# Kernel tuning notes

Hardware: AMD Instinct MI355X
Metric: run time of the kernel (lower is better)

Reference implementation:

```python
import jax, jax.numpy as jnp
import numpy as np

B, L, D, N_HEADS = 8, 512, 1024, 16
D_HEAD = D // N_HEADS


def _mha_fuzzy(x_q, x_k, x_v, Wq, bq, Wk, bk, Wv, bv, Wo, bo):
    """Multi-head fuzzy attention, product t-norm score function."""
    b, lq, d_model = x_q.shape
    lk = x_k.shape[1]

    def proj(x, W, bias, l):
        # [b, l, D] -> [b, h, l, d_head]
        return (x @ W + bias).reshape(b, l, N_HEADS, D_HEAD).transpose(0, 2, 1, 3)

    Q = proj(x_q, Wq, bq, lq)
    K = proj(x_k, Wk, bk, lk)
    V = proj(x_v, Wv, bv, lk)
    # fuzzy memberships in [0,1]
    mu_q = jax.nn.sigmoid(Q)
    mu_k = jax.nn.sigmoid(K)
    # product t-norm aggregated over feature dim (mean), then softmax normalize
    scores = jnp.einsum('bhid,bhjd->bhij', mu_q, mu_k) / D_HEAD  # [b,h,lq,lk]
    attn = jax.nn.softmax(scores, axis=-1)
    out = jnp.einsum('bhij,bhjd->bhid', attn, V)
    out = out.transpose(0, 2, 1, 3).reshape(b, lq, d_model)
    return out @ Wo + bo, attn.mean(axis=1)  # avg over heads


def setup_inputs() -> dict:
    key = jax.random.key(0)
    ks = jax.random.split(key, 16)
    s = 1.0 / np.sqrt(D)
    inp = {
        'text_features': jax.random.normal(ks[0], (B, L, D), jnp.float32),
        'image_features': jax.random.normal(ks[1], (B, L, D), jnp.float32),
        'Wq': jax.random.normal(ks[2], (D, D), jnp.float32) * s,
        'bq': jnp.zeros((D,), jnp.float32),
        'Wk': jax.random.normal(ks[3], (D, D), jnp.float32) * s,
        'bk': jnp.zeros((D,), jnp.float32),
        'Wv': jax.random.normal(ks[4], (D, D), jnp.float32) * s,
        'bv': jnp.zeros((D,), jnp.float32),
        'Wo': jax.random.normal(ks[5], (D, D), jnp.float32) * s,
        'bo': jnp.zeros((D,), jnp.float32),
        'W1': jax.random.normal(ks[6], (3 * D, D), jnp.float32) * (1.0 / np.sqrt(3 * D)),
        'b1': jnp.zeros((D,), jnp.float32),
        'W2': jax.random.normal(ks[7], (D, D), jnp.float32) * s,
        'b2': jnp.zeros((D,), jnp.float32),
    }
    return inp


def reference(text_features, image_features, Wq, bq, Wk, bk, Wv, bv, Wo, bo, W1, b1, W2, b2):
    # shared fuzzy attention module applied in both cross-modal directions
    text_cross, avg_attn = _mha_fuzzy(text_features, image_features, image_features,
                                      Wq, bq, Wk, bk, Wv, bv, Wo, bo)
    image_cross, _ = _mha_fuzzy(image_features, text_features, text_features,
                                Wq, bq, Wk, bk, Wv, bv, Wo, bo)
    combined = jnp.concatenate([text_features, image_features, text_cross], axis=-1)
    hidden = jax.nn.relu(combined @ W1 + b1)
    compositional_output = hidden @ W2 + b2
    return text_cross, image_cross, compositional_output, avg_attn
```

## Files before the change

kernel.cpp:

```cpp
#include <hip/hip_runtime.h>

#define NB 8
#define SL 512
#define DM 1024
#define NH 16
#define DH 64

using bfrag = __attribute__((ext_vector_type(8))) short;
using facc  = __attribute__((ext_vector_type(4))) float;

__device__ __forceinline__ float bf2f(ushort u) {
    return __uint_as_float(((unsigned)u) << 16);
}
__device__ __forceinline__ ushort f2bf(float f) {
    unsigned x = __float_as_uint(f);
    return (ushort)((x + 0x7FFFu + ((x >> 16) & 1u)) >> 16);
}
__device__ __forceinline__ float4 bf4_f4(ushort4 u) {
    return make_float4(bf2f(u.x), bf2f(u.y), bf2f(u.z), bf2f(u.w));
}
__device__ __forceinline__ unsigned pack2(float a, float b) {
    return (unsigned)f2bf(a) | ((unsigned)f2bf(b) << 16);
}
__device__ __forceinline__ void gload16(const ushort* g, ushort* l) {
    __builtin_amdgcn_global_load_lds(
        (const __attribute__((address_space(1))) unsigned*)g,
        (__attribute__((address_space(3))) unsigned*)l, 16, 0, 0);
}

__global__ __launch_bounds__(256)
void cvt_k(const float* __restrict__ s, ushort* __restrict__ d) {
    const size_t i = (size_t)(blockIdx.x * 256 + threadIdx.x) * 4;
    const float4 f = *(const float4*)(s + i);
    *(ushort4*)(d + i) = make_ushort4(f2bf(f.x), f2bf(f.y), f2bf(f.z), f2bf(f.w));
}

__global__ __launch_bounds__(256)
void tconv_k(const float* __restrict__ W, ushort* __restrict__ WT,
             const int R, const int C) {
    __shared__ ushort T[64][68];
    const int tid = threadIdx.x;
    const int c0 = blockIdx.x * 64, r0 = blockIdx.y * 64;
    #pragma unroll
    for (int rr = 0; rr < 4; ++rr) {
        const int r = (tid >> 4) + rr * 16;
        const int c4 = (tid & 15) * 4;
        const float4 f = *(const float4*)(W + (size_t)(r0 + r) * C + c0 + c4);
        T[c4+0][r] = f2bf(f.x); T[c4+1][r] = f2bf(f.y);
        T[c4+2][r] = f2bf(f.z); T[c4+3][r] = f2bf(f.w);
    }
    __syncthreads();
    #pragma unroll
    for (int rr = 0; rr < 4; ++rr) {
        const int c = (tid >> 4) + rr * 16;
        const int r4 = (tid & 15) * 4;
        *(ushort4*)(WT + (size_t)(c0 + c) * R + r0 + r4) =
            make_ushort4(T[c][r4+0], T[c][r4+1], T[c][r4+2], T[c][r4+3]);
    }
}

template<int ACT, int OMODE>
__global__ __launch_bounds__(256, 2)
void mfma_gemm(const ushort* __restrict__ A0, const ushort* __restrict__ A1,
               const float* __restrict__ A2f,
               const int KA1, const int KA2, const int Ktot,
               const int lda, const int ldaf,
               const ushort* __restrict__ AM1, const int Msplit,
               const ushort* __restrict__ BT, const int ldb,
               const float* __restrict__ bias, const float* __restrict__ biasK,
               const float* __restrict__ biasV,
               float* __restrict__ outf, ushort* __restrict__ outb,
               ushort* __restrict__ outbK, ushort* __restrict__ outbVT,
               const int clustN)
{
    __shared__ ushort sh[32768];
    const int tid  = threadIdx.x;
    const int w    = tid >> 6;
    const int lane = tid & 63;
    const int ln   = lane & 15, qd = lane >> 4;
    const int wm = (w & 1) * 64, wn = (w >> 1) * 64;

    const int NTg = gridDim.x, MTg = gridDim.y;
    const int L   = blockIdx.x + NTg * blockIdx.y;
    const int xcd = L & 7, sIdx = L >> 3;
    int mt, nt;
    if (clustN) { const int np = NTg >> 3; nt = xcd * np + sIdx % np; mt = sIdx / np; }
    else        { mt = xcd * (MTg >> 3) + sIdx / NTg; nt = sIdx - (sIdx / NTg) * NTg; }
    const int m0 = mt * 128, n0 = nt * 128;

    const ushort* A0u = A0; const ushort* A1u = A1; int m0A = m0;
    if (Msplit && m0 >= Msplit) { A0u = AM1; A1u = AM1; m0A = m0 - Msplit; }

    const int arow = (lane >> 3);
    const int kc8s = ((lane & 7) ^ arow) * 8;

    facc acc[4][4];
    #pragma unroll
    for (int i = 0; i < 4; ++i)
        #pragma unroll
        for (int j = 0; j < 4; ++j)
            acc[i][j] = (facc){0.f, 0.f, 0.f, 0.f};

    auto stage = [&](int k0, ushort* buf) {
        ushort* Asb = buf;
        ushort* Bsb = buf + 8192;
        #pragma unroll
        for (int t = 0; t < 4; ++t) {
            const int c = w * 4 + t;
            gload16(BT + (size_t)(n0 + c * 8 + arow) * ldb + k0 + kc8s,
                    &Bsb[c * 512]);
        }
        if (k0 < KA2) {
            const ushort* Ab; int ko;
            if (k0 < KA1) { Ab = A0u; ko = k0; }
            else          { Ab = A1u; ko = k0 - KA1; }
            #pragma unroll
            for (int t = 0; t < 4; ++t) {
                const int c = w * 4 + t;
                gload16(Ab + (size_t)(m0A + c * 8 + arow) * lda + ko + kc8s,
                        &Asb[c * 512]);
            }
        } else {
            const int ko = k0 - KA2;
            #pragma unroll
            for (int t = 0; t < 4; ++t) {
                const int c = w * 4 + t;
                const float* src = A2f + (size_t)(m0A + c * 8 + arow) * ldaf + ko + kc8s;
                const float4 f0 = *(const float4*)src;
                const float4 f1 = *(const float4*)(src + 4);
                uint4 p;
                p.x = pack2(f0.x, f0.y); p.y = pack2(f0.z, f0.w);
                p.z = pack2(f1.x, f1.y); p.w = pack2(f1.z, f1.w);
                *(uint4*)&Asb[c * 512 + lane * 8] = p;
            }
        }
    };

    stage(0, sh);
    for (int k0 = 0; k0 < Ktot; k0 += 64) {
        ushort* cur = sh + ((k0 >> 6) & 1) * 16384;
        ushort* nxt = sh + (((k0 >> 6) & 1) ^ 1) * 16384;
        __syncthreads();
        if (k0 + 64 < Ktot) stage(k0 + 64, nxt);
        ushort* Asb = cur;
        ushort* Bsb = cur + 8192;
        #pragma unroll
        for (int ks = 0; ks < 2; ++ks) {
            const int ch = (ks * 4 + qd) ^ (ln & 7);
            bfrag af[4], bfv[4];
            #pragma unroll
            for (int i = 0; i < 4; ++i)
                af[i] = *(const bfrag*)&Asb[(wm + i*16 + ln) * 64 + ch * 8];
            #pragma unroll
            for (int j = 0; j < 4; ++j)
                bfv[j] = *(const bfrag*)&Bsb[(wn + j*16 + ln) * 64 + ch * 8];
            #pragma unroll
            for (int i = 0; i < 4; ++i)
                #pragma unroll
                for (int j = 0; j < 4; ++j)
                    acc[i][j] = __builtin_amdgcn_mfma_f32_16x16x32_bf16(
                        af[i], bfv[j], acc[i][j], 0, 0, 0);
        }
    }

    if (OMODE == 4) {
        const int seg   = n0 >> 10;
        const int nloc0 = n0 & 1023;
        const float* bs = (seg == 0) ? bias : (seg == 1) ? biasK : biasV;
        if (seg < 2) {
            ushort* ob = (seg == 0) ? outb : outbK;
            #pragma unroll
            for (int j = 0; j < 4; ++j) {
                const int nl = nloc0 + wn + j * 16 + ln;
                const float bn = bs[nl];
                #pragma unroll
                for (int i = 0; i < 4; ++i) {
                    const int mb = m0 + wm + i * 16 + qd * 4;
                    #pragma unroll
                    for (int r = 0; r < 4; ++r) {
                        const float v = 1.f / (1.f + __expf(-(acc[i][j][r] + bn)));
                        const int m = mb + r;
                        const int g = m >> 9, l = m & 511;
                        ob[(((size_t)(g * NH + (nl >> 6))) * SL + l) * DH + (nl & 63)]
                            = f2bf(v);
                    }
                }
            }
        } else {
            __syncthreads();
            #pragma unroll
            for (int j = 0; j < 4; ++j) {
                const int n_l = wn + j * 16 + ln;
                const float bn = bs[nloc0 + n_l];
                #pragma unroll
                for (int i = 0; i < 4; ++i) {
                    #pragma unroll
                    for (int r = 0; r < 4; ++r) {
                        const int m_l = wm + i * 16 + qd * 4 + r;
                        const int c = (m_l >> 3) ^ (n_l & 7);
                        sh[n_l * 128 + c * 8 + (m_l & 7)] = f2bf(acc[i][j][r] + bn);
                    }
                }
            }
            __syncthreads();
            const int n_l = tid >> 1, half = tid & 1;
            const int nl = nloc0 + n_l;
            const int g = m0 >> 9, l0 = m0 & 511;
            ushort* dst = outbVT +
                (((size_t)(g * NH + (nl >> 6))) * DH + (nl & 63)) * SL + l0;
            #pragma unroll
            for (int u = 0; u < 8; ++u) {
                const int c = half * 8 + u;
                const int cs = c ^ (n_l & 7);
                *(uint4*)(dst + c * 8) = *(const uint4*)&sh[n_l * 128 + cs * 8];
            }
        }
        return;
    }

    #pragma unroll
    for (int j = 0; j < 4; ++j) {
        const int n = n0 + wn + j * 16 + ln;
        const float bn = bias[n];
        #pragma unroll
        for (int i = 0; i < 4; ++i) {
            const int mb = m0 + wm + i * 16 + qd * 4;
            #pragma unroll
            for (int r = 0; r < 4; ++r) {
                float v = acc[i][j][r] + bn;
                if (ACT == 1)      v = 1.f / (1.f + __expf(-v));
                else if (ACT == 2) v = v > 0.f ? v : 0.f;
                const int m = mb + r;
                if (OMODE == 0) outf[(size_t)m * DM + n] = v;
                else            outb[(size_t)m * DM + n] = f2bf(v);
            }
        }
    }
}

__global__ __launch_bounds__(256, 2)
void attn2_k(const ushort* __restrict__ Qm, const ushort* __restrict__ Km,
             const ushort* __restrict__ VTm, ushort* __restrict__ AO,
             float* __restrict__ RS)
{
    __shared__ ushort Ks[128 * 64];
    __shared__ ushort VTs[64 * 128];
    __shared__ ushort Es[128 * 128];
    const int tid  = threadIdx.x;
    const int w    = tid >> 6;
    const int lane = tid & 63;
    const int ln   = lane & 15, qd = lane >> 4;
    const int wm  = (w & 1) * 64;
    const int wns = (w >> 1) * 64;
    const int wnd = (w >> 1) * 32;
    const int qt = blockIdx.x, h = blockIdx.y, b = blockIdx.z;
    const size_t ho = ((size_t)(b * NH + h)) * SL * DH;
    const ushort* Qg  = Qm  + ho + (size_t)qt * 128 * DH;
    const ushort* Kg  = Km  + ho;
    const ushort* VTg = VTm + ho;

    bfrag qf[4][2];
    #pragma unroll
    for (int i = 0; i < 4; ++i)
        #pragma unroll
        for (int ks = 0; ks < 2; ++ks)
            qf[i][ks] = *(const bfrag*)(Qg + (size_t)(wm + i*16 + ln) * DH + ks*32 + qd*8);

    facc oacc[4][2];
    #pragma unroll
    for (int i = 0; i < 4; ++i)
        #pragma unroll
        for (int j = 0; j < 2; ++j)
            oacc[i][j] = (facc){0.f, 0.f, 0.f, 0.f};
    float rp[4][4];
    #pragma unroll
    for (int i = 0; i < 4; ++i)
        #pragma unroll
        for (int r = 0; r < 4; ++r)
            rp[i][r] = 0.f;

    const int arow = lane >> 3;
    const int kc8s = ((lane & 7) ^ arow) * 8;
    const int vrow = lane >> 4;

    for (int kc = 0; kc < 4; ++kc) {
        __syncthreads();
        #pragma unroll
        for (int t = 0; t < 4; ++t) {
            const int c = w * 4 + t;
            const int vc8s = ((lane & 15) ^ ((c * 4 + vrow) & 7)) * 8;
            gload16(Kg + (size_t)(kc*128 + c*8 + arow) * DH + kc8s, &Ks[c * 512]);
            gload16(VTg + (size_t)(c*4 + vrow) * SL + kc*128 + vc8s, &VTs[c * 512]);
        }
        __syncthreads();

        facc sacc[4][4];
        #pragma unroll
        for (int i = 0; i < 4; ++i)
            #pragma unroll
            for (int j = 0; j < 4; ++j)
                sacc[i][j] = (facc){0.f, 0.f, 0.f, 0.f};
        #pragma unroll
        for (int ks = 0; ks < 2; ++ks) {
            const int ch = (ks * 4 + qd) ^ (ln & 7);
            bfrag kf[4];
            #pragma unroll
            for (int j = 0; j < 4; ++j)
                kf[j] = *(const bfrag*)&Ks[(wns + j*16 + ln) * 64 + ch * 8];
            #pragma unroll
            for (int i = 0; i < 4; ++i)
                #pragma unroll
                for (int j = 0; j < 4; ++j)
                    sacc[i][j] = __builtin_amdgcn_mfma_f32_16x16x32_bf16(
                        qf[i][ks], kf[j], sacc[i][j], 0, 0, 0);
        }

        #pragma unroll
        for (int i = 0; i < 4; ++i) {
            #pragma unroll
            for (int r = 0; r < 4; ++r) {
                const int q = wm + i*16 + qd*4 + r;
                float p = 0.f;
                #pragma unroll
                for (int j = 0; j < 4; ++j) {
                    const float e = __expf(sacc[i][j][r] * 0.015625f);
                    const int key = wns + j*16 + ln;
                    const int c = (key >> 3) ^ (q & 7);
                    Es[q * 128 + c * 8 + (key & 7)] = f2bf(e);
                    p += e;
                }
                p += __shfl_xor(p, 1, 16);
                p += __shfl_xor(p, 2, 16);
                p += __shfl_xor(p, 4, 16);
                p += __shfl_xor(p, 8, 16);
                rp[i][r] += p;
            }
        }
        __syncthreads();

        #pragma unroll
        for (int ks2 = 0; ks2 < 4; ++ks2) {
            const int vch = (ks2 * 4 + qd) ^ (ln & 7);
            bfrag ea[4], vb[2];
            #pragma unroll
            for (int i = 0; i < 4; ++i) {
                const int q = wm + i*16 + ln;
                const int cs = (ks2*4 + qd) ^ (q & 7);
                ea[i] = *(const bfrag*)&Es[q * 128 + cs * 8];
            }
            #pragma unroll
            for (int j = 0; j < 2; ++j)
                vb[j] = *(const bfrag*)&VTs[(wnd + j*16 + ln) * 128 + vch * 8];
            #pragma unroll
            for (int i = 0; i < 4; ++i)
                #pragma unroll
                for (int j = 0; j < 2; ++j)
                    oacc[i][j] = __builtin_amdgcn_mfma_f32_16x16x32_bf16(
                        ea[i], vb[j], oacc[i][j], 0, 0, 0);
        }
    }

    __syncthreads();
    float* rsls = (float*)Ks;
    if (ln == 0) {
        #pragma unroll
        for (int i = 0; i < 4; ++i)
            #pragma unroll
            for (int r = 0; r < 4; ++r)
                rsls[(w >> 1) * 128 + wm + i*16 + qd*4 + r] = rp[i][r];
    }
    __syncthreads();
    if (tid < 128) {
        const float t = rsls[tid] + rsls[128 + tid];
        RS[(size_t)(b * NH + h) * SL + qt * 128 + tid] = t;
        rsls[tid] = t;
    }
    __syncthreads();

    #pragma unroll
    for (int i = 0; i < 4; ++i) {
        #pragma unroll
        for (int r = 0; r < 4; ++r) {
            const int q = wm + i*16 + qd*4 + r;
            const float inv = 1.f / rsls[q];
            const size_t rowo = ((size_t)(b*SL + qt*128 + q)) * DM + h*DH;
            #pragma unroll
            for (int j = 0; j < 2; ++j)
                AO[rowo + wnd + j*16 + ln] = f2bf(oacc[i][j][r] * inv);
        }
    }
}

__global__ __launch_bounds__(256, 2)
void avg3_k(const ushort* __restrict__ Qm, const ushort* __restrict__ Km,
            const float* __restrict__ RS, float* __restrict__ avga)
{
    __shared__ ushort Qs[64 * 64];
    __shared__ ushort Kt[64 * 64];
    __shared__ float rss[64];
    const int tid  = threadIdx.x;
    const int w    = tid >> 6;
    const int lane = tid & 63;
    const int ln   = lane & 15, qd = lane >> 4;
    const int wq = (w & 1) * 32, wk = (w >> 1) * 32;
    const int kt = blockIdx.x, qt = blockIdx.y, b = blockIdx.z;

    const int arow = lane >> 3;
    const int kc8s = ((lane & 7) ^ arow) * 8;

    float acc[2][2][4];
    #pragma unroll
    for (int i = 0; i < 2; ++i)
        #pragma unroll
        for (int j = 0; j < 2; ++j)
            #pragma unroll
            for (int r = 0; r < 4; ++r)
                acc[i][j][r] = 0.f;

    for (int h = 0; h < NH; ++h) {
        const size_t ho = ((size_t)(b * NH + h)) * SL * DH;
        __syncthreads();
        #pragma unroll
        for (int t = 0; t < 2; ++t) {
            const int c = w * 2 + t;
            gload16(Qm + ho + (size_t)(qt*64 + c*8 + arow) * DH + kc8s, &Qs[c * 512]);
            gload16(Km + ho + (size_t)(kt*64 + c*8 + arow) * DH + kc8s, &Kt[c * 512]);
        }
        if (tid < 64) rss[tid] = RS[(size_t)(b*NH + h)*SL + qt*64 + tid];
        __syncthreads();

        facc s[2][2];
        #pragma unroll
        for (int i = 0; i < 2; ++i)
            #pragma unroll
            for (int j = 0; j < 2; ++j)
                s[i][j] = (facc){0.f, 0.f, 0.f, 0.f};
        #pragma unroll
        for (int ks = 0; ks < 2; ++ks) {
            const int ch = (ks * 4 + qd) ^ (ln & 7);
            bfrag qa[2], kb[2];
            #pragma unroll
            for (int i = 0; i < 2; ++i)
                qa[i] = *(const bfrag*)&Qs[(wq + i*16 + ln) * 64 + ch * 8];
            #pragma unroll
            for (int j = 0; j < 2; ++j)
                kb[j] = *(const bfrag*)&Kt[(wk + j*16 + ln) * 64 + ch * 8];
            #pragma unroll
            for (int i = 0; i < 2; ++i)
                #pragma unroll
                for (int j = 0; j < 2; ++j)
                    s[i][j] = __builtin_amdgcn_mfma_f32_16x16x32_bf16(
                        qa[i], kb[j], s[i][j], 0, 0, 0);
        }
        #pragma unroll
        for (int i = 0; i < 2; ++i) {
            #pragma unroll
            for (int r = 0; r < 4; ++r) {
                const float ir = 0.0625f / rss[wq + i*16 + qd*4 + r];
                #pragma unroll
                for (int j = 0; j < 2; ++j)
                    acc[i][j][r] += __expf(s[i][j][r] * 0.015625f) * ir;
            }
        }
    }
    #pragma unroll
    for (int i = 0; i < 2; ++i) {
        #pragma unroll
        for (int r = 0; r < 4; ++r) {
            const int q = wq + i*16 + qd*4 + r;
            #pragma unroll
            for (int j = 0; j < 2; ++j)
                avga[((size_t)(b*SL + qt*64 + q)) * SL + kt*64 + wk + j*16 + ln]
                    = acc[i][j][r];
        }
    }
}

extern "C" void kernel_launch(void* const* d_in, const int* in_sizes, int n_in,
                              void* d_out, int out_size, void* d_ws, size_t ws_size,
                              hipStream_t stream)
{
    (void)in_sizes; (void)n_in; (void)out_size; (void)ws_size;
    const float* text  = (const float*)d_in[0];
    const float* image = (const float*)d_in[1];
    const float* Wq = (const float*)d_in[2];
    const float* bq = (const float*)d_in[3];
    const float* Wk = (const float*)d_in[4];
    const float* bk = (const float*)d_in[5];
    const float* Wv = (const float*)d_in[6];
    const float* bv = (const float*)d_in[7];
    const float* Wo = (const float*)d_in[8];
    const float* bo = (const float*)d_in[9];
    const float* W1 = (const float*)d_in[10];
    const float* b1 = (const float*)d_in[11];
    const float* W2 = (const float*)d_in[12];
    const float* b2 = (const float*)d_in[13];
    float* out = (float*)d_out;

    const size_t SZ   = (size_t)NB * SL * DM;
    const size_t HALF = SZ;

    ushort* xbf = (ushort*)d_ws;
    ushort* Qb  = xbf + 2*SZ;
    ushort* Kb  = Qb  + 2*SZ;
    ushort* VT  = Kb  + 2*SZ;
    ushort* AOt = VT  + 2*SZ;
    ushort* Wt  = AOt + SZ;
    float*  RS  = (float*)(Wt + 3*DM*DM);
    ushort* AOi    = VT + HALF;
    ushort* hidden = Qb;

    float* text_cross = out;
    float* comp       = out + 2*SZ;
    float* avga       = out + 3*SZ;

    const dim3 blk(256);

    cvt_k<<<4096, blk, 0, stream>>>(text,  xbf);
    cvt_k<<<4096, blk, 0, stream>>>(image, xbf + SZ);

    tconv_k<<<dim3(16,16), blk, 0, stream>>>(Wq, Wt,           DM, DM);
    tconv_k<<<dim3(16,16), blk, 0, stream>>>(Wk, Wt + DM*DM,   DM, DM);
    tconv_k<<<dim3(16,16), blk, 0, stream>>>(Wv, Wt + 2*DM*DM, DM, DM);
    mfma_gemm<0,4><<<dim3(24,64), blk, 0, stream>>>(
        xbf, xbf, nullptr, DM, DM, DM, DM, DM, nullptr, 0,
        Wt, DM, bq, bk, bv, nullptr, Qb, Kb, VT, 1);

    attn2_k<<<dim3(SL/128, NH, NB), blk, 0, stream>>>(Qb, Kb + HALF, VT + HALF, AOt, RS);
    avg3_k<<<dim3(SL/64, SL/64, NB), blk, 0, stream>>>(Qb, Kb + HALF, RS, avga);
    attn2_k<<<dim3(SL/128, NH, NB), blk, 0, stream>>>(Qb + HALF, Kb, VT, AOi, RS);

    tconv_k<<<dim3(16,16), blk, 0, stream>>>(Wo, Wt, DM, DM);
    mfma_gemm<0,0><<<dim3(8,64), blk, 0, stream>>>(
        AOt, AOt, nullptr, DM, DM, DM, DM, DM, AOi, 4096,
        Wt, DM, bo, nullptr, nullptr, text_cross, nullptr, nullptr, nullptr, 0);

    tconv_k<<<dim3(16,48), blk, 0, stream>>>(W1, Wt, 3*DM, DM);
    mfma_gemm<2,2><<<dim3(8,32), blk, 0, stream>>>(
        xbf, xbf + SZ, text_cross, DM, 2*DM, 3*DM, DM, DM, nullptr, 0,
        Wt, 3*DM, b1, nullptr, nullptr, nullptr, hidden, nullptr, nullptr, 0);
    tconv_k<<<dim3(16,16), blk, 0, stream>>>(W2, Wt, DM, DM);
    mfma_gemm<0,0><<<dim3(8,32), blk, 0, stream>>>(
        hidden, hidden, nullptr, DM, DM, DM, DM, DM, nullptr, 0,
        Wt, DM, b2, nullptr, nullptr, comp, nullptr, nullptr, nullptr, 0);
}
```

Before: 401.1 us.

## Merge weight transposes into one launch and fuse fp32 activation conversion into GEMMs

All six weight transpose-and-convert launches are replaced by a single 3D-grid kernel that writes every transposed bf16 weight to its own workspace slot. The separate fp32-to-bf16 conversion kernels for text and image are removed. The QKV and W1 GEMMs now read fp32 activations directly and convert them while staging into LDS. This cuts kernel launches and a round trip of bf16 activations through memory, but those GEMMs lose the async global-to-LDS load path and do the conversion in registers, reading twice the bytes per tile and converting repeatedly across N tiles.

```diff
diff --git a/kernel.cpp b/kernel.cpp
--- a/kernel.cpp
+++ b/kernel.cpp
@@ -16,9 +16,6 @@
     unsigned x = __float_as_uint(f);
     return (ushort)((x + 0x7FFFu + ((x >> 16) & 1u)) >> 16);
 }
-__device__ __forceinline__ float4 bf4_f4(ushort4 u) {
-    return make_float4(bf2f(u.x), bf2f(u.y), bf2f(u.z), bf2f(u.w));
-}
 __device__ __forceinline__ unsigned pack2(float a, float b) {
     return (unsigned)f2bf(a) | ((unsigned)f2bf(b) << 16);
 }
@@ -29,15 +26,23 @@
 }
 
 __global__ __launch_bounds__(256)
-void cvt_k(const float* __restrict__ s, ushort* __restrict__ d) {
-    const size_t i = (size_t)(blockIdx.x * 256 + threadIdx.x) * 4;
-    const float4 f = *(const float4*)(s + i);
-    *(ushort4*)(d + i) = make_ushort4(f2bf(f.x), f2bf(f.y), f2bf(f.z), f2bf(f.w));
-}
-
-__global__ __launch_bounds__(256)
-void tconv_k(const float* __restrict__ W, ushort* __restrict__ WT,
-             const int R, const int C) {
+void tconv_all(const float* __restrict__ Wq, const float* __restrict__ Wk,
+               const float* __restrict__ Wv, const float* __restrict__ Wo,
+               const float* __restrict__ W1, const float* __restrict__ W2,
+               ushort* __restrict__ Wt)
+{
+    const int z = blockIdx.z;
+    if (z != 4 && blockIdx.y >= 16) return;
+    const float* W; ushort* WT; int R;
+    const int D2 = DM * DM;
+    switch (z) {
+        case 0:  W = Wq; WT = Wt;          R = DM;     break;
+        case 1:  W = Wk; WT = Wt + D2;     R = DM;     break;
+        case 2:  W = Wv; WT = Wt + 2*D2;   R = DM;     break;
+        case 3:  W = Wo; WT = Wt + 3*D2;   R = DM;     break;
+        case 4:  W = W1; WT = Wt + 4*D2;   R = 3*DM;   break;
+        default: W = W2; WT = Wt + 7*D2;   R = DM;     break;
+    }
     __shared__ ushort T[64][68];
     const int tid = threadIdx.x;
     const int c0 = blockIdx.x * 64, r0 = blockIdx.y * 64;
@@ -45,7 +50,7 @@
     for (int rr = 0; rr < 4; ++rr) {
         const int r = (tid >> 4) + rr * 16;
         const int c4 = (tid & 15) * 4;
-        const float4 f = *(const float4*)(W + (size_t)(r0 + r) * C + c0 + c4);
+        const float4 f = *(const float4*)(W + (size_t)(r0 + r) * DM + c0 + c4);
         T[c4+0][r] = f2bf(f.x); T[c4+1][r] = f2bf(f.y);
         T[c4+2][r] = f2bf(f.z); T[c4+3][r] = f2bf(f.w);
     }
@@ -59,13 +64,12 @@
     }
 }
 
-template<int ACT, int OMODE>
+template<int ACT, int OMODE, int AFP32>
 __global__ __launch_bounds__(256, 2)
-void mfma_gemm(const ushort* __restrict__ A0, const ushort* __restrict__ A1,
-               const float* __restrict__ A2f,
-               const int KA1, const int KA2, const int Ktot,
-               const int lda, const int ldaf,
-               const ushort* __restrict__ AM1, const int Msplit,
+void mfma_gemm(const ushort* __restrict__ A0, const ushort* __restrict__ AM1,
+               const float* __restrict__ F0, const float* __restrict__ F1,
+               const float* __restrict__ F2, const float* __restrict__ FM1,
+               const int KA1, const int KA2, const int Ktot, const int Msplit,
                const ushort* __restrict__ BT, const int ldb,
                const float* __restrict__ bias, const float* __restrict__ biasK,
                const float* __restrict__ biasV,
@@ -88,8 +92,10 @@
     else        { mt = xcd * (MTg >> 3) + sIdx / NTg; nt = sIdx - (sIdx / NTg) * NTg; }
     const int m0 = mt * 128, n0 = nt * 128;
 
-    const ushort* A0u = A0; const ushort* A1u = A1; int m0A = m0;
-    if (Msplit && m0 >= Msplit) { A0u = AM1; A1u = AM1; m0A = m0 - Msplit; }
+    const ushort* A0u = A0;
+    const float*  F0u = F0;
+    int m0A = m0;
+    if (Msplit && m0 >= Msplit) { A0u = AM1; F0u = FM1; m0A = m0 - Msplit; }
 
     const int arow = (lane >> 3);
     const int kc8s = ((lane & 7) ^ arow) * 8;
@@ -110,28 +116,28 @@
             gload16(BT + (size_t)(n0 + c * 8 + arow) * ldb + k0 + kc8s,
                     &Bsb[c * 512]);
         }
-        if (k0 < KA2) {
-            const ushort* Ab; int ko;
-            if (k0 < KA1) { Ab = A0u; ko = k0; }
-            else          { Ab = A1u; ko = k0 - KA1; }
+        if (AFP32) {
+            const float* src; int ko;
+            if (k0 < KA1)      { src = F0u; ko = k0; }
+            else if (k0 < KA2) { src = F1;  ko = k0 - KA1; }
+            else               { src = F2;  ko = k0 - KA2; }
             #pragma unroll
             for (int t = 0; t < 4; ++t) {
                 const int c = w * 4 + t;
-                gload16(Ab + (size_t)(m0A + c * 8 + arow) * lda + ko + kc8s,
-                        &Asb[c * 512]);
-            }
-        } else {
-            const int ko = k0 - KA2;
-            #pragma unroll
-            for (int t = 0; t < 4; ++t) {
-                const int c = w * 4 + t;
-                const float* src = A2f + (size_t)(m0A + c * 8 + arow) * ldaf + ko + kc8s;
-                const float4 f0 = *(const float4*)src;
-                const float4 f1 = *(const float4*)(src + 4);
+                const float* s = src + (size_t)(m0A + c * 8 + arow) * DM + ko + kc8s;
+                const float4 f0 = *(const float4*)s;
+                const float4 f1 = *(const float4*)(s + 4);
                 uint4 p;
                 p.x = pack2(f0.x, f0.y); p.y = pack2(f0.z, f0.w);
                 p.z = pack2(f1.x, f1.y); p.w = pack2(f1.z, f1.w);
                 *(uint4*)&Asb[c * 512 + lane * 8] = p;
+            }
+        } else {
+            #pragma unroll
+            for (int t = 0; t < 4; ++t) {
+                const int c = w * 4 + t;
+                gload16(A0u + (size_t)(m0A + c * 8 + arow) * DM + k0 + kc8s,
+                        &Asb[c * 512]);
             }
         }
     };
@@ -499,14 +505,14 @@
 
     const size_t SZ   = (size_t)NB * SL * DM;
     const size_t HALF = SZ;
-
-    ushort* xbf = (ushort*)d_ws;
-    ushort* Qb  = xbf + 2*SZ;
+    const size_t D2   = (size_t)DM * DM;
+
+    ushort* Qb  = (ushort*)d_ws;
     ushort* Kb  = Qb  + 2*SZ;
     ushort* VT  = Kb  + 2*SZ;
     ushort* AOt = VT  + 2*SZ;
     ushort* Wt  = AOt + SZ;
-    float*  RS  = (float*)(Wt + 3*DM*DM);
+    float*  RS  = (float*)(Wt + 8*D2);
     ushort* AOi    = VT + HALF;
     ushort* hidden = Qb;
 
@@ -516,31 +522,27 @@
 
     const dim3 blk(256);
 
-    cvt_k<<<4096, blk, 0, stream>>>(text,  xbf);
-    cvt_k<<<4096, blk, 0, stream>>>(image, xbf + SZ);
-
-    tconv_k<<<dim3(16,16), blk, 0, stream>>>(Wq, Wt,           DM, DM);
-    tconv_k<<<dim3(16,16), blk, 0, stream>>>(Wk, Wt + DM*DM,   DM, DM);
-    tconv_k<<<dim3(16,16), blk, 0, stream>>>(Wv, Wt + 2*DM*DM, DM, DM);
-    mfma_gemm<0,4><<<dim3(24,64), blk, 0, stream>>>(
-        xbf, xbf, nullptr, DM, DM, DM, DM, DM, nullptr, 0,
-        Wt, DM, bq, bk, bv, nullptr, Qb, Kb, VT, 1);
+    tconv_all<<<dim3(16, 48, 6), blk, 0, stream>>>(Wq, Wk, Wv, Wo, W1, W2, Wt);
+
+    mfma_gemm<0,4,1><<<dim3(24,64), blk, 0, stream>>>(
+        nullptr, nullptr, text, nullptr, nullptr, image,
+        DM, DM, DM, 4096, Wt, DM, bq, bk, bv, nullptr, Qb, Kb, VT, 1);
 
     attn2_k<<<dim3(SL/128, NH, NB), blk, 0, stream>>>(Qb, Kb + HALF, VT + HALF, AOt, RS);
     avg3_k<<<dim3(SL/64, SL/64, NB), blk, 0, stream>>>(Qb, Kb + HALF, RS, avga);
     attn2_k<<<dim3(SL/128, NH, NB), blk, 0, stream>>>(Qb + HALF, Kb, VT, AOi, RS);
 
-    tconv_k<<<dim3(16,16), blk, 0, stream>>>(Wo, Wt, DM, DM);
-    mfma_gemm<0,0><<<dim3(8,64), blk, 0, stream>>>(
-        AOt, AOt, nullptr, DM, DM, DM, DM, DM, AOi, 4096,
-        Wt, DM, bo, nullptr, nullptr, text_cross, nullptr, nullptr, nullptr, 0);
-
-    tconv_k<<<dim3(16,48), blk, 0, stream>>>(W1, Wt, 3*DM, DM);
-    mfma_gemm<2,2><<<dim3(8,32), blk, 0, stream>>>(
-        xbf, xbf + SZ, text_cross, DM, 2*DM, 3*DM, DM, DM, nullptr, 0,
-        Wt, 3*DM, b1, nullptr, nullptr, nullptr, hidden, nullptr, nullptr, 0);
-    tconv_k<<<dim3(16,16), blk, 0, stream>>>(W2, Wt, DM, DM);
-    mfma_gemm<0,0><<<dim3(8,32), blk, 0, stream>>>(
-        hidden, hidden, nullptr, DM, DM, DM, DM, DM, nullptr, 0,
-        Wt, DM, b2, nullptr, nullptr, comp, nullptr, nullptr, nullptr, 0);
-}
+    mfma_gemm<0,0,0><<<dim3(8,64), blk, 0, stream>>>(
+        AOt, AOi, nullptr, nullptr, nullptr, nullptr,
+        DM, DM, DM, 4096, Wt + 3*D2, DM, bo, nullptr, nullptr,
+        text_cross, nullptr, nullptr, nullptr, 0);
+
+    mfma_gemm<2,2,1><<<dim3(8,32), blk, 0, stream>>>(
+        nullptr, nullptr, text, image, text_cross, nullptr,
+        DM, 2*DM, 3*DM, 0, Wt + 4*D2, 3*DM, b1, nullptr, nullptr,
+        nullptr, hidden, nullptr, nullptr, 0);
+    mfma_gemm<0,0,0><<<dim3(8,32), blk, 0, stream>>>(
+        hidden, nullptr, nullptr, nullptr, nullptr, nullptr,
+        DM, DM, DM, 0, Wt + 7*D2, DM, b2, nullptr, nullptr,
+        comp, nullptr, nullptr, nullptr, 0);
+}
```

Measured after the change: 435.5 us. 8.6% more time.
